# Kernel tuning notes

Measured on AMD Instinct MI355X. Metric: run time of the kernel, lower is better.

## Reference

```python
import jax, jax.numpy as jnp
import numpy as np

NUM_HEADS = 16


def setup_inputs() -> dict:
    key = jax.random.key(0)
    k1, k2, k3, k4 = jax.random.split(key, 4)
    B, S, D = 2, 2048, 1024
    x = jax.random.normal(k1, (B, S, D), dtype=jnp.float32)
    W_qkv = jax.random.normal(k2, (D, 3 * D), dtype=jnp.float32) * (1.0 / np.sqrt(D))
    b_qkv = jax.random.normal(k3, (3 * D,), dtype=jnp.float32) * 0.02
    W_out = jax.random.normal(k4, (D, D), dtype=jnp.float32) * (1.0 / np.sqrt(D))
    return {"x": x, "W_qkv": W_qkv, "b_qkv": b_qkv, "W_out": W_out}


def reference(x, W_qkv, b_qkv, W_out):
    B, S, D = x.shape
    H = NUM_HEADS
    Hd = D // H
    scale = 1.0 / np.sqrt(Hd)

    qkv = x @ W_qkv + b_qkv                      # [B, S, 3D]
    q, k, v = jnp.split(qkv, 3, axis=-1)
    # [B, H, S, Hd]
    q = q.reshape(B, S, H, Hd).transpose(0, 2, 1, 3)
    k = k.reshape(B, S, H, Hd).transpose(0, 2, 1, 3)
    v = v.reshape(B, S, H, Hd).transpose(0, 2, 1, 3)

    scores = jnp.einsum('bhqd,bhkd->bhqk', q, k) * scale  # [B, H, S, S]
    causal = jnp.triu(jnp.full((S, S), -jnp.inf, dtype=scores.dtype), k=1)
    scores = scores + causal
    attn = jax.nn.softmax(scores.astype(jnp.float32), axis=-1).astype(q.dtype)

    ctx = jnp.einsum('bhqk,bhkd->bhqd', attn, v)           # [B, H, S, Hd]
    ctx = ctx.transpose(0, 2, 1, 3).reshape(B, S, D)
    return ctx @ W_out
```

## Files before the change

kernel.cpp:

```cpp
#include <hip/hip_runtime.h>
#include <hip/hip_bf16.h>

typedef __bf16 bf16x8 __attribute__((ext_vector_type(8)));
typedef float f32x4 __attribute__((ext_vector_type(4)));

typedef __attribute__((address_space(1))) void gv_t;
typedef __attribute__((address_space(3))) void lv_t;

__device__ __forceinline__ unsigned short f2bf(float f) {
    unsigned int u = __float_as_uint(f);
    unsigned int r = (u + 0x7fffu + ((u >> 16) & 1u)) >> 16;
    return (unsigned short)r;
}

__device__ __forceinline__ unsigned int cvt_pk_bf16(float a, float b) {
    unsigned int r;
    asm("v_cvt_pk_bf16_f32 %0, %1, %2" : "=v"(r) : "v"(a), "v"(b));
    return r;
}

__global__ void convert_f32_bf16(const float* __restrict__ in,
                                 unsigned short* __restrict__ out, int n4) {
    int i = blockIdx.x * blockDim.x + threadIdx.x;
    if (i >= n4) return;
    float4 v = reinterpret_cast<const float4*>(in)[i];
    ushort4 o;
    o.x = f2bf(v.x); o.y = f2bf(v.y); o.z = f2bf(v.z); o.w = f2bf(v.w);
    reinterpret_cast<ushort4*>(out)[i] = o;
}

__global__ void transpose_convert(const float* __restrict__ in,
                                  unsigned short* __restrict__ out,
                                  int K, int N) {
    __shared__ float t[32][33];
    int n0 = blockIdx.x * 32, k0 = blockIdx.y * 32;
    t[threadIdx.y][threadIdx.x] = in[(size_t)(k0 + threadIdx.y) * N + (n0 + threadIdx.x)];
    __syncthreads();
    out[(size_t)(n0 + threadIdx.y) * K + (k0 + threadIdx.x)] = f2bf(t[threadIdx.x][threadIdx.y]);
}

template <bool BIAS, bool OUT_BF16, bool QSCALE>
__global__ __launch_bounds__(256) void gemm_bt(const unsigned short* __restrict__ A,
                                               const unsigned short* __restrict__ Bt,
                                               const float* __restrict__ bias,
                                               void* __restrict__ Cv,
                                               int M, int N, int K) {
    __shared__ alignas(16) unsigned short As[128 * 32];
    __shared__ alignas(16) unsigned short Bs[128 * 32];

    const int t = threadIdx.x;
    const int lane = t & 63;
    const int wid = t >> 6;
    const int wr = wid >> 1, wc = wid & 1;
    const int m0 = blockIdx.y * 128, n0 = blockIdx.x * 128;

    f32x4 acc[4][4] = {};

    for (int k0 = 0; k0 < K; k0 += 32) {
#pragma unroll
        for (int i = 0; i < 2; ++i) {
            int c = i * 256 + t;
            int row = c >> 2;
            int col = (c & 3) * 8;
            const unsigned short* ga = A + (size_t)(m0 + row) * K + k0 + col;
            const unsigned short* gb = Bt + (size_t)(n0 + row) * K + k0 + col;
            __builtin_amdgcn_global_load_lds((gv_t*)ga, (lv_t*)(As + c * 8), 16, 0, 0);
            __builtin_amdgcn_global_load_lds((gv_t*)gb, (lv_t*)(Bs + c * 8), 16, 0, 0);
        }
        __syncthreads();

        bf16x8 af[4], bfr[4];
#pragma unroll
        for (int i = 0; i < 4; ++i)
            af[i] = *reinterpret_cast<const bf16x8*>(As + (wr * 64 + i * 16 + (lane & 15)) * 32 + (lane >> 4) * 8);
#pragma unroll
        for (int j = 0; j < 4; ++j)
            bfr[j] = *reinterpret_cast<const bf16x8*>(Bs + (wc * 64 + j * 16 + (lane & 15)) * 32 + (lane >> 4) * 8);
#pragma unroll
        for (int i = 0; i < 4; ++i)
#pragma unroll
            for (int j = 0; j < 4; ++j)
                acc[i][j] = __builtin_amdgcn_mfma_f32_16x16x32_bf16(af[i], bfr[j], acc[i][j], 0, 0, 0);
        __syncthreads();
    }

#pragma unroll
    for (int i = 0; i < 4; ++i) {
        int row = m0 + wr * 64 + i * 16 + (lane >> 4) * 4;
#pragma unroll
        for (int j = 0; j < 4; ++j) {
            int col = n0 + wc * 64 + j * 16 + (lane & 15);
            float bv = 0.0f;
            if (BIAS) bv = bias[col];
#pragma unroll
            for (int r = 0; r < 4; ++r) {
                float v = acc[i][j][r] + bv;
                if constexpr (QSCALE) { if (col < 1024) v *= 0.125f; }
                if constexpr (OUT_BF16)
                    ((unsigned short*)Cv)[(size_t)(row + r) * N + col] = f2bf(v);
                else
                    ((float*)Cv)[(size_t)(row + r) * N + col] = v;
            }
        }
    }
}

__global__ __launch_bounds__(256) void attn_fwd(const unsigned short* __restrict__ qkv,
                                                unsigned short* __restrict__ ctx,
                                                int S) {
    const int TD = 3072, D = 1024;
    __shared__ alignas(16) unsigned short Ks[2][64 * 64];
    __shared__ alignas(16) unsigned short Vt[2][64 * 64];
    __shared__ alignas(16) unsigned short Ps[4][16 * 64];

    const int t = threadIdx.x, lane = t & 63, w = t >> 6;
    const int l15 = lane & 15, l4 = lane >> 4;
    const int pid = blockIdx.x;
    const int bh = blockIdx.y;
    const int b = bh >> 4, h = bh & 15;
    const int QT_lo = pid, QT_hi = 31 - pid;

    const size_t base = ((size_t)b * S) * TD + (size_t)h * 64;
    const unsigned short* qp = qkv + base;
    const unsigned short* kp = qkv + base + D;
    const unsigned short* vp = qkv + base + 2 * D;

    bf16x8 aq_hi[2], aq_lo[2];
    {
        const unsigned short* gh = qp + (size_t)(QT_hi * 64 + w * 16 + l15) * TD + l4 * 8;
        aq_hi[0] = *reinterpret_cast<const bf16x8*>(gh);
        aq_hi[1] = *reinterpret_cast<const bf16x8*>(gh + 32);
        const unsigned short* gl = qp + (size_t)(QT_lo * 64 + w * 16 + l15) * TD + l4 * 8;
        aq_lo[0] = *reinterpret_cast<const bf16x8*>(gl);
        aq_lo[1] = *reinterpret_cast<const bf16x8*>(gl + 32);
    }

    f32x4 oc_hi[4] = {}, oc_lo[4] = {};
    float m_hi = -1e30f, l_hi = 0.f, m_lo = -1e30f, l_lo = 0.f;

    const float L2E = 1.44269504f;

    auto stageK = [&](int j0, int buf) {
#pragma unroll
        for (int rnd = 0; rnd < 2; ++rnd) {
            int c = rnd * 256 + t;
            int row = c >> 3, hh = c & 7;
            const unsigned short* src = kp + (size_t)(j0 * 64 + row) * TD + ((hh ^ (row & 7)) * 8);
            __builtin_amdgcn_global_load_lds((gv_t*)src, (lv_t*)(Ks[buf] + c * 8), 16, 0, 0);
        }
    };
    const int v_hd = (t & 31) * 2, v_kvb = (t >> 5) * 8;
    unsigned int vv[8];
    auto loadV = [&](int j0) {
        const unsigned short* vsrc = vp + (size_t)(j0 * 64 + v_kvb) * TD + v_hd;
#pragma unroll
        for (int e = 0; e < 8; ++e)
            vv[e] = *reinterpret_cast<const unsigned int*>(vsrc + (size_t)e * TD);
    };
    auto writeV = [&](int buf) {
        unsigned int r0[4], r1[4];
#pragma unroll
        for (int i = 0; i < 4; ++i) {
            r0[i] = __builtin_amdgcn_perm(vv[2 * i + 1], vv[2 * i], 0x05040100u);
            r1[i] = __builtin_amdgcn_perm(vv[2 * i + 1], vv[2 * i], 0x07060302u);
        }
        int g0 = (v_kvb >> 3) ^ (v_hd & 7);
        int g1 = (v_kvb >> 3) ^ ((v_hd + 1) & 7);
        *reinterpret_cast<uint4*>(Vt[buf] + v_hd * 64 + g0 * 8) = make_uint4(r0[0], r0[1], r0[2], r0[3]);
        *reinterpret_cast<uint4*>(Vt[buf] + (v_hd + 1) * 64 + g1 * 8) = make_uint4(r1[0], r1[1], r1[2], r1[3]);
    };

    auto compute = [&](const bf16x8* aq, f32x4* oc, float& mR, float& lR, bool diag, int buf) {
        f32x4 sc[4];
        __builtin_amdgcn_s_setprio(1);
#pragma unroll
        for (int jn = 0; jn < 4; ++jn) {
            f32x4 s = {};
#pragma unroll
            for (int kk = 0; kk < 2; ++kk) {
                int row = jn * 16 + l15;
                int g = (kk * 4 + l4) ^ (l15 & 7);
                bf16x8 ak = *reinterpret_cast<const bf16x8*>(Ks[buf] + row * 64 + g * 8);
                s = __builtin_amdgcn_mfma_f32_16x16x32_bf16(ak, aq[kk], s, 0, 0, 0);
            }
            sc[jn] = s;
        }
        __builtin_amdgcn_s_setprio(0);
        if (diag) {
            int ql = w * 16 + l15;
#pragma unroll
            for (int jn = 0; jn < 4; ++jn)
#pragma unroll
                for (int r = 0; r < 4; ++r)
                    if (jn * 16 + l4 * 4 + r > ql) sc[jn][r] = -1e30f;
        }
        float pm = -1e30f;
#pragma unroll
        for (int jn = 0; jn < 4; ++jn) {
            float a = fmaxf(sc[jn][0], sc[jn][1]);
            float c = fmaxf(sc[jn][2], sc[jn][3]);
            pm = fmaxf(pm, fmaxf(a, c));
        }
        pm = fmaxf(pm, __shfl_xor(pm, 16));
        pm = fmaxf(pm, __shfl_xor(pm, 32));
        float mnew = fmaxf(mR, pm);
        float alpha = exp2f((mR - mnew) * L2E);
        float mn2 = mnew * L2E;
        float ps = 0.f;
#pragma unroll
        for (int jn = 0; jn < 4; ++jn) {
            float p0 = exp2f(sc[jn][0] * L2E - mn2);
            float p1 = exp2f(sc[jn][1] * L2E - mn2);
            float p2 = exp2f(sc[jn][2] * L2E - mn2);
            float p3 = exp2f(sc[jn][3] * L2E - mn2);
            sc[jn][0] = p0; sc[jn][1] = p1; sc[jn][2] = p2; sc[jn][3] = p3;
            ps += (p0 + p1) + (p2 + p3);
        }
        ps += __shfl_xor(ps, 16);
        ps += __shfl_xor(ps, 32);
        lR = lR * alpha + ps;
        mR = mnew;
#pragma unroll
        for (int jc = 0; jc < 4; ++jc) oc[jc] *= alpha;
        const int q = l15;
#pragma unroll
        for (int jn = 0; jn < 4; ++jn) {
            unsigned int lo = cvt_pk_bf16(sc[jn][0], sc[jn][1]);
            unsigned int hi = cvt_pk_bf16(sc[jn][2], sc[jn][3]);
            int kv0 = jn * 16 + l4 * 4;
            int g = (kv0 >> 3) ^ (q & 7);
            *reinterpret_cast<uint2*>(Ps[w] + q * 64 + g * 8 + (kv0 & 7)) = make_uint2(lo, hi);
        }
        __builtin_amdgcn_s_setprio(1);
#pragma unroll
        for (int kk = 0; kk < 2; ++kk) {
            int gq = (kk * 4 + l4) ^ (q & 7);
            bf16x8 bp = *reinterpret_cast<const bf16x8*>(Ps[w] + q * 64 + gq * 8);
#pragma unroll
            for (int jc = 0; jc < 4; ++jc) {
                int hdrow = jc * 16 + l15;
                int gv = (kk * 4 + l4) ^ (l15 & 7);
                bf16x8 av = *reinterpret_cast<const bf16x8*>(Vt[buf] + hdrow * 64 + gv * 8);
                oc[jc] = __builtin_amdgcn_mfma_f32_16x16x32_bf16(av, bp, oc[jc], 0, 0, 0);
            }
        }
        __builtin_amdgcn_s_setprio(0);
    };

    stageK(0, 0);
    loadV(0);
    writeV(0);
    __syncthreads();

    for (int j0 = 0; j0 <= QT_hi; ++j0) {
        const int cur = j0 & 1, nxt = cur ^ 1;
        const bool have_next = (j0 < QT_hi);
        if (have_next) {
            stageK(j0 + 1, nxt);
            loadV(j0 + 1);
        }
        compute(aq_hi, oc_hi, m_hi, l_hi, j0 == QT_hi, cur);
        if (j0 <= QT_lo) compute(aq_lo, oc_lo, m_lo, l_lo, j0 == QT_lo, cur);
        if (have_next) writeV(nxt);
        __syncthreads();
    }

    auto epi = [&](f32x4* oc, float lR, int QT) {
        float inv = 1.0f / lR;
        size_t qg = (size_t)QT * 64 + w * 16 + l15;
        unsigned short* crow = ctx + ((size_t)b * S + qg) * D + h * 64;
#pragma unroll
        for (int jc = 0; jc < 4; ++jc) {
            unsigned int pk0 = cvt_pk_bf16(oc[jc][0] * inv, oc[jc][1] * inv);
            unsigned int pk1 = cvt_pk_bf16(oc[jc][2] * inv, oc[jc][3] * inv);
            *reinterpret_cast<uint2*>(crow + jc * 16 + l4 * 4) = make_uint2(pk0, pk1);
        }
    };
    epi(oc_hi, l_hi, QT_hi);
    epi(oc_lo, l_lo, QT_lo);
}

extern "C" void kernel_launch(void* const* d_in, const int* in_sizes, int n_in,
                              void* d_out, int out_size, void* d_ws, size_t ws_size,
                              hipStream_t stream) {
    const float* x = (const float*)d_in[0];
    const float* Wqkv = (const float*)d_in[1];
    const float* bqkv = (const float*)d_in[2];
    const float* Wout = (const float*)d_in[3];
    float* out = (float*)d_out;

    const int B = 2, S = 2048, D = 1024, TD = 3072;
    const int M = B * S;

    char* ws = (char*)d_ws;
    unsigned short* x_bf  = (unsigned short*)(ws);
    unsigned short* wqkvT = (unsigned short*)(ws + 8388608);
    unsigned short* woutT = (unsigned short*)(ws + 14680064);
    unsigned short* qkv   = (unsigned short*)(ws + 16777216);
    unsigned short* ctx   = (unsigned short*)(ws + 41943040);

    convert_f32_bf16<<<dim3((M * D / 4 + 255) / 256), dim3(256), 0, stream>>>(x, x_bf, M * D / 4);
    transpose_convert<<<dim3(TD / 32, D / 32), dim3(32, 32), 0, stream>>>(Wqkv, wqkvT, D, TD);
    transpose_convert<<<dim3(D / 32, D / 32), dim3(32, 32), 0, stream>>>(Wout, woutT, D, D);

    gemm_bt<true, true, true><<<dim3(TD / 128, M / 128), dim3(256), 0, stream>>>(
        x_bf, wqkvT, bqkv, (void*)qkv, M, TD, D);

    attn_fwd<<<dim3(16, 32), dim3(256), 0, stream>>>(qkv, ctx, S);

    gemm_bt<false, false, false><<<dim3(D / 128, M / 128), dim3(256), 0, stream>>>(
        ctx, woutT, nullptr, (void*)out, M, D, D);
}
```

Measured before the change: 143.8 us.

## Give each attention block one query tile and add lazy softmax rescaling

The attention kernel stops pairing a low and a high causal query tile in one block. It now launches 32 blocks per head, each handling one query tile, with the longest tiles scheduled first. The online softmax also skips rescaling of the running max, sum and accumulators unless some lane's new max exceeds the old one by more than 8. This doubles the grid for more parallelism but gives up the K/V tile reuse shared by the two tiles. The lazy rescale avoids exp and multiply work, at the cost of exponentials up to 2^8 times larger, which is safe in fp32.

After: 160.9 us. 1.12x slower.

```diff
diff --git a/kernel.cpp b/kernel.cpp
--- a/kernel.cpp
+++ b/kernel.cpp
@@ -115,28 +115,24 @@
 
     const int t = threadIdx.x, lane = t & 63, w = t >> 6;
     const int l15 = lane & 15, l4 = lane >> 4;
-    const int pid = blockIdx.x;
+    const int qt = 31 - (int)blockIdx.x;
     const int bh = blockIdx.y;
     const int b = bh >> 4, h = bh & 15;
-    const int QT_lo = pid, QT_hi = 31 - pid;
 
     const size_t base = ((size_t)b * S) * TD + (size_t)h * 64;
     const unsigned short* qp = qkv + base;
     const unsigned short* kp = qkv + base + D;
     const unsigned short* vp = qkv + base + 2 * D;
 
-    bf16x8 aq_hi[2], aq_lo[2];
+    bf16x8 aq[2];
     {
-        const unsigned short* gh = qp + (size_t)(QT_hi * 64 + w * 16 + l15) * TD + l4 * 8;
-        aq_hi[0] = *reinterpret_cast<const bf16x8*>(gh);
-        aq_hi[1] = *reinterpret_cast<const bf16x8*>(gh + 32);
-        const unsigned short* gl = qp + (size_t)(QT_lo * 64 + w * 16 + l15) * TD + l4 * 8;
-        aq_lo[0] = *reinterpret_cast<const bf16x8*>(gl);
-        aq_lo[1] = *reinterpret_cast<const bf16x8*>(gl + 32);
-    }
-
-    f32x4 oc_hi[4] = {}, oc_lo[4] = {};
-    float m_hi = -1e30f, l_hi = 0.f, m_lo = -1e30f, l_lo = 0.f;
+        const unsigned short* g = qp + (size_t)(qt * 64 + w * 16 + l15) * TD + l4 * 8;
+        aq[0] = *reinterpret_cast<const bf16x8*>(g);
+        aq[1] = *reinterpret_cast<const bf16x8*>(g + 32);
+    }
+
+    f32x4 oc[4] = {};
+    float mR = -1e30f, lR = 0.f;
 
     const float L2E = 1.44269504f;
 
@@ -170,7 +166,7 @@
         *reinterpret_cast<uint4*>(Vt[buf] + (v_hd + 1) * 64 + g1 * 8) = make_uint4(r1[0], r1[1], r1[2], r1[3]);
     };
 
-    auto compute = [&](const bf16x8* aq, f32x4* oc, float& mR, float& lR, bool diag, int buf) {
+    auto compute = [&](bool diag, int buf) {
         f32x4 sc[4];
         __builtin_amdgcn_s_setprio(1);
 #pragma unroll
@@ -196,16 +192,20 @@
         }
         float pm = -1e30f;
 #pragma unroll
-        for (int jn = 0; jn < 4; ++jn) {
-            float a = fmaxf(sc[jn][0], sc[jn][1]);
-            float c = fmaxf(sc[jn][2], sc[jn][3]);
-            pm = fmaxf(pm, fmaxf(a, c));
-        }
+        for (int jn = 0; jn < 4; ++jn)
+            pm = fmaxf(fmaxf(pm, fmaxf(sc[jn][0], sc[jn][1])),
+                       fmaxf(sc[jn][2], sc[jn][3]));
         pm = fmaxf(pm, __shfl_xor(pm, 16));
         pm = fmaxf(pm, __shfl_xor(pm, 32));
-        float mnew = fmaxf(mR, pm);
-        float alpha = exp2f((mR - mnew) * L2E);
-        float mn2 = mnew * L2E;
+        if (__any(pm > mR + 8.0f)) {
+            float mnew = fmaxf(mR, pm);
+            float alpha = exp2f((mR - mnew) * L2E);
+            mR = mnew;
+            lR *= alpha;
+#pragma unroll
+            for (int jc = 0; jc < 4; ++jc) oc[jc] *= alpha;
+        }
+        float mn2 = mR * L2E;
         float ps = 0.f;
 #pragma unroll
         for (int jn = 0; jn < 4; ++jn) {
@@ -218,10 +218,7 @@
         }
         ps += __shfl_xor(ps, 16);
         ps += __shfl_xor(ps, 32);
-        lR = lR * alpha + ps;
-        mR = mnew;
-#pragma unroll
-        for (int jc = 0; jc < 4; ++jc) oc[jc] *= alpha;
+        lR += ps;
         const int q = l15;
 #pragma unroll
         for (int jn = 0; jn < 4; ++jn) {
@@ -252,22 +249,21 @@
     writeV(0);
     __syncthreads();
 
-    for (int j0 = 0; j0 <= QT_hi; ++j0) {
+    for (int j0 = 0; j0 <= qt; ++j0) {
         const int cur = j0 & 1, nxt = cur ^ 1;
-        const bool have_next = (j0 < QT_hi);
+        const bool have_next = (j0 < qt);
         if (have_next) {
             stageK(j0 + 1, nxt);
             loadV(j0 + 1);
         }
-        compute(aq_hi, oc_hi, m_hi, l_hi, j0 == QT_hi, cur);
-        if (j0 <= QT_lo) compute(aq_lo, oc_lo, m_lo, l_lo, j0 == QT_lo, cur);
+        compute(j0 == qt, cur);
         if (have_next) writeV(nxt);
         __syncthreads();
     }
 
-    auto epi = [&](f32x4* oc, float lR, int QT) {
+    {
         float inv = 1.0f / lR;
-        size_t qg = (size_t)QT * 64 + w * 16 + l15;
+        size_t qg = (size_t)qt * 64 + w * 16 + l15;
         unsigned short* crow = ctx + ((size_t)b * S + qg) * D + h * 64;
 #pragma unroll
         for (int jc = 0; jc < 4; ++jc) {
@@ -275,9 +271,7 @@
             unsigned int pk1 = cvt_pk_bf16(oc[jc][2] * inv, oc[jc][3] * inv);
             *reinterpret_cast<uint2*>(crow + jc * 16 + l4 * 4) = make_uint2(pk0, pk1);
         }
-    };
-    epi(oc_hi, l_hi, QT_hi);
-    epi(oc_lo, l_lo, QT_lo);
+    }
 }
 
 extern "C" void kernel_launch(void* const* d_in, const int* in_sizes, int n_in,
@@ -306,7 +300,7 @@
     gemm_bt<true, true, true><<<dim3(TD / 128, M / 128), dim3(256), 0, stream>>>(
         x_bf, wqkvT, bqkv, (void*)qkv, M, TD, D);
 
-    attn_fwd<<<dim3(16, 32), dim3(256), 0, stream>>>(qkv, ctx, S);
+    attn_fwd<<<dim3(32, 32), dim3(256), 0, stream>>>(qkv, ctx, S);
 
     gemm_bt<false, false, false><<<dim3(D / 128, M / 128), dim3(256), 0, stream>>>(
         ctx, woutT, nullptr, (void*)out, M, D, D);
```
